# Kernel optimization log

Measured on AMD Instinct MI355X. Metric: run time of the kernel, lower is better.

The kernel has to match this reference:

```python
import jax, jax.numpy as jnp
import numpy as np

D_MODEL = 1024
NUM_HEADS = 16
DEPTH = D_MODEL // NUM_HEADS  # 64
BATCH, SEQ = 4, 2048


def setup_inputs() -> dict:
    key = jax.random.key(0)
    ks = jax.random.split(key, 9)
    s = 1.0 / np.sqrt(D_MODEL)
    x = jax.random.normal(ks[0], (BATCH, SEQ, D_MODEL), dtype=jnp.float32)
    # Per-head Dense weights stacked on a leading head axis [H, d_model, depth]
    Wq = jax.random.normal(ks[1], (NUM_HEADS, D_MODEL, DEPTH), dtype=jnp.float32) * s
    Wk = jax.random.normal(ks[2], (NUM_HEADS, D_MODEL, DEPTH), dtype=jnp.float32) * s
    Wv = jax.random.normal(ks[3], (NUM_HEADS, D_MODEL, DEPTH), dtype=jnp.float32) * s
    bq = jnp.zeros((NUM_HEADS, DEPTH), dtype=jnp.float32)
    bk = jnp.zeros((NUM_HEADS, DEPTH), dtype=jnp.float32)
    bv = jnp.zeros((NUM_HEADS, DEPTH), dtype=jnp.float32)
    Wo = jax.random.normal(ks[4], (D_MODEL, D_MODEL), dtype=jnp.float32) * s
    bo = jnp.zeros((D_MODEL,), dtype=jnp.float32)
    return {"x": x, "Wq": Wq, "bq": bq, "Wk": Wk, "bk": bk,
            "Wv": Wv, "bv": bv, "Wo": Wo, "bo": bo}


def reference(x, Wq, bq, Wk, bk, Wv, bv, Wo, bo):
    # Batched equivalent of the per-head loop: project, attend, concat heads.
    q = jnp.einsum('bsd,hde->bhse', x, Wq) + bq[:, None, :]  # [B,H,S,depth]
    k = jnp.einsum('bsd,hde->bhse', x, Wk) + bk[:, None, :]
    v = jnp.einsum('bsd,hde->bhse', x, Wv) + bv[:, None, :]
    scale = 1.0 / jnp.sqrt(jnp.asarray(DEPTH, dtype=x.dtype))
    scores = jnp.einsum('bhse,bhte->bhst', q, k) * scale      # [B,H,S,S]
    weights = jax.nn.softmax(scores, axis=-1)
    heads = jnp.einsum('bhst,bhte->bhse', weights, v)         # [B,H,S,depth]
    # concat head outputs along last axis in head order (tf.concat axis=-1)
    multi = jnp.transpose(heads, (0, 2, 1, 3)).reshape(x.shape[0], x.shape[1], D_MODEL)
    return multi @ Wo + bo
```

## Files before the change

kernel.cpp:

```cpp
#include <hip/hip_runtime.h>
#include <hip/hip_bf16.h>

#define BATCH 4
#define SEQ   2048
#define DM    1024
#define NH    16
#define DEPTH 64
#define ROWS  (BATCH*SEQ)
#define NQKV  (3*DM)
#define BH    (BATCH*NH)

typedef __attribute__((ext_vector_type(8))) short bf16x8;
typedef __attribute__((ext_vector_type(4))) float f32x4;
typedef __attribute__((ext_vector_type(16))) float f32x16;
typedef unsigned short u16;
typedef unsigned int   u32;

__device__ __forceinline__ u16 f2bf(float f) {
    union { float f; unsigned u; } v; v.f = f;
    unsigned r = v.u + 0x7fff + ((v.u >> 16) & 1);
    return (u16)(r >> 16);
}

__device__ __forceinline__ u32 pk2bf(float a, float b) {
#if __has_builtin(__builtin_amdgcn_cvt_pk_bf16_f32)
    typedef __attribute__((ext_vector_type(2))) __bf16 v2bf;
    union { v2bf v; u32 u; } u_;
    u_.v = __builtin_amdgcn_cvt_pk_bf16_f32(a, b);
    return u_.u;
#else
    return (u32)f2bf(a) | ((u32)f2bf(b) << 16);
#endif
}

__device__ __forceinline__ void plswap(u32 a, u32 b, u32& x, u32& y) {
#if __has_builtin(__builtin_amdgcn_permlane32_swap)
    typedef __attribute__((ext_vector_type(2))) int i32x2;
    i32x2 r = __builtin_amdgcn_permlane32_swap((int)a, (int)b, false, false);
    x = (u32)r.x; y = (u32)r.y;
#else
    u32 as = (u32)__shfl_xor((int)a, 32);
    u32 bs = (u32)__shfl_xor((int)b, 32);
    int h = (threadIdx.x >> 5) & 1;
    x = h ? bs : a;
    y = h ? b : as;
#endif
}

__device__ __forceinline__ void g2l16(void* lds, const void* g) {
    __builtin_amdgcn_global_load_lds((const __attribute__((address_space(1))) void*)g,
                                     (__attribute__((address_space(3))) void*)lds, 16, 0, 0);
}

__device__ __forceinline__ bf16x8 frag8(const u16* tile, int row, int gl) {
    return *(const bf16x8*)(tile + row * 64 + ((gl ^ (row & 7)) * 8));
}

__device__ __forceinline__ f32x16 mfma32(bf16x8 a, bf16x8 b, f32x16 c) {
    return __builtin_amdgcn_mfma_f32_32x32x16_bf16(a, b, c, 0, 0, 0);
}

__global__ __launch_bounds__(256) void k_prep(const float* __restrict__ x,
                                              const float* __restrict__ Wq, const float* __restrict__ Wk,
                                              const float* __restrict__ Wv, const float* __restrict__ Wo,
                                              u16* __restrict__ xb, u16* __restrict__ BT, u16* __restrict__ WoT) {
    __shared__ u16 T[64][65];
    int tid = threadIdx.x;
    int bx = blockIdx.x;
    if (bx < 2048) {
        int i = bx * 4096 + tid * 4;
        for (int l = 0; l < 4; ++l) {
            float4 v = *(const float4*)(x + i + l * 1024);
            ushort4 o; o.x = f2bf(v.x); o.y = f2bf(v.y); o.z = f2bf(v.z); o.w = f2bf(v.w);
            *(ushort4*)(xb + i + l * 1024) = o;
        }
        return;
    }
    if (bx < 2816) {
        int q = bx - 2048;
        int kt = q & 15, mh = q >> 4, m = mh >> 4, h = mh & 15;
        const float* W = (m == 0) ? Wq : (m == 1) ? Wk : Wv;
        const float* src = W + ((size_t)h * 1024 + kt * 64) * 64;
        int e = tid & 63, r0 = tid >> 6;
        for (int i = 0; i < 16; ++i) { int r = i * 4 + r0; T[r][e] = f2bf(src[r * 64 + e]); }
        __syncthreads();
        int kk = tid & 63, e0 = tid >> 6;
        u16* dst = BT + ((size_t)m * 1024 + h * 64) * 1024 + kt * 64;
        for (int i = 0; i < 16; ++i) { int ee = i * 4 + e0; dst[ee * 1024 + kk] = T[kk][ee]; }
        return;
    }
    {
        int q = bx - 2816;
        int kt = q & 15, nt = q >> 4;
        const float* src = Wo + (size_t)kt * 64 * 1024 + nt * 64;
        int c = tid & 63, r0 = tid >> 6;
        for (int i = 0; i < 16; ++i) { int r = i * 4 + r0; T[r][c] = f2bf(src[r * 1024 + c]); }
        __syncthreads();
        int kk = tid & 63, e0 = tid >> 6;
        u16* dst = WoT + (size_t)nt * 64 * 1024 + kt * 64;
        for (int i = 0; i < 16; ++i) { int ee = i * 4 + e0; dst[ee * 1024 + kk] = T[kk][ee]; }
    }
}

__global__ __launch_bounds__(256) void k_gemm_qkv(const u16* __restrict__ xb, const u16* __restrict__ Wt,
                                                  const float* __restrict__ bq, const float* __restrict__ bk,
                                                  const float* __restrict__ bv,
                                                  u16* __restrict__ Q, u16* __restrict__ K, u16* __restrict__ VT) {
    __shared__ u16 Al[128 * 64];
    __shared__ u16 Bl[128 * 64];
    int tid = threadIdx.x;
    int wave = tid >> 6, lane = tid & 63, ln = lane & 15, quad = lane >> 4;
    int b = blockIdx.x;
    bool isvt = (b >= 1024);
    int row0, col0;
    const u16 *Am, *Bm;
    if (!isvt) {
        col0 = (b & 15) * 128; row0 = (b >> 4) * 128;
        Am = xb + (size_t)row0 * 1024; Bm = Wt + (size_t)col0 * 1024;
    } else {
        int b2 = b - 1024;
        col0 = (b2 & 63) * 128; row0 = (b2 >> 6) * 128;
        Am = Wt + (size_t)2048 * 1024 + (size_t)row0 * 1024; Bm = xb + (size_t)col0 * 1024;
    }
    int moff = (wave >> 1) * 64, noff = (wave & 1) * 64;
    f32x4 acc[4][4] = {};

    for (int k0 = 0; k0 < 1024; k0 += 64) {
        for (int l = 0; l < 4; ++l) {
            int idx = tid + l * 256, r = idx >> 3, gs = ((idx & 7) ^ (r & 7)) * 8;
            g2l16(&Al[idx * 8], Am + r * 1024 + k0 + gs);
            g2l16(&Bl[idx * 8], Bm + r * 1024 + k0 + gs);
        }
        __syncthreads();
        for (int kk = 0; kk < 2; ++kk) {
            bf16x8 a[4], bb[4];
            for (int i = 0; i < 4; ++i) a[i]  = frag8(Al, moff + i * 16 + ln, kk * 4 + quad);
            for (int j = 0; j < 4; ++j) bb[j] = frag8(Bl, noff + j * 16 + ln, kk * 4 + quad);
            for (int i = 0; i < 4; ++i)
                for (int j = 0; j < 4; ++j)
                    acc[i][j] = __builtin_amdgcn_mfma_f32_16x16x32_bf16(a[i], bb[j], acc[i][j], 0, 0, 0);
        }
        __syncthreads();
    }

    if (!isvt) {
        const float QSCALE = 0.125f * 1.4426950408889634f;
        for (int j = 0; j < 4; ++j) {
            int c = col0 + noff + j * 16 + ln;
            int m = c >> 10, h = (c >> 6) & 15, e = c & 63;
            const float* bias = (m == 0) ? bq : bk;
            float bval = bias[h * 64 + e];
            for (int i = 0; i < 4; ++i)
                for (int r = 0; r < 4; ++r) {
                    int rowg = row0 + moff + i * 16 + quad * 4 + r;
                    int b_ = rowg >> 11, s = rowg & 2047;
                    int bh = b_ * 16 + h;
                    float v = acc[i][j][r] + bval;
                    if (m == 0) Q[(bh * 2048 + s) * 64 + e] = f2bf(v * QSCALE);
                    else        K[(bh * 2048 + s) * 64 + e] = f2bf(v);
                }
        }
    } else {
        for (int j = 0; j < 4; ++j) {
            int c = col0 + noff + j * 16 + ln;
            int b_ = c >> 11, s = c & 2047;
            for (int i = 0; i < 4; ++i)
                for (int r = 0; r < 4; ++r) {
                    int ii = row0 + moff + i * 16 + quad * 4 + r;
                    float v = acc[i][j][r] + bv[ii];
                    VT[((size_t)b_ * 1024 + ii) * 2048 + s] = f2bf(v);
                }
        }
    }
}

__global__ __launch_bounds__(256, 4) void k_attn(const u16* __restrict__ Q, const u16* __restrict__ K,
                                                 const u16* __restrict__ VT, u16* __restrict__ A2) {
    __shared__ u16 Kl[2][64 * 64];
    __shared__ u16 Vl[2][64 * 64];
    __shared__ float linv[128];
    int tid = threadIdx.x;
    int wave = tid >> 6, lane = tid & 63, l31 = lane & 31, h = lane >> 5;
    int bh = blockIdx.y;
    int m0 = blockIdx.x * 128;
    const u16* Qb = Q + (size_t)bh * 2048 * 64;
    const u16* Kb = K + (size_t)bh * 2048 * 64;
    const u16* Vb = VT + (size_t)bh * 64 * 2048;

    const u16* kp[2]; const u16* vp[2]; int dsti[2];
    for (int l = 0; l < 2; ++l) {
        int idx = tid + l * 256, r = idx >> 3, gs = ((idx & 7) ^ (r & 7)) * 8;
        dsti[l] = idx * 8;
        kp[l] = Kb + r * 64 + gs;
        vp[l] = Vb + r * 2048 + gs;
    }

    bf16x8 qb[4];
    {
        const u16* q0 = Qb + (size_t)(m0 + wave * 32 + l31) * 64 + h * 8;
#pragma unroll
        for (int s = 0; s < 4; ++s) qb[s] = *(const bf16x8*)(q0 + s * 16);
    }

    for (int l = 0; l < 2; ++l) { g2l16(&Kl[0][dsti[l]], kp[l]); g2l16(&Vl[0][dsti[l]], vp[l]); }
    __syncthreads();

    f32x16 oacc[2] = {};
    float lsum = 0.f;

    for (int t = 0; t < 32; ++t) {
        int cur = t & 1;
        if (t < 31) {
            for (int l = 0; l < 2; ++l) {
                g2l16(&Kl[cur ^ 1][dsti[l]], kp[l] + (t + 1) * 4096);
                g2l16(&Vl[cur ^ 1][dsti[l]], vp[l] + (t + 1) * 64);
            }
        }

        f32x16 sc[2] = {};
        __builtin_amdgcn_s_setprio(1);
#pragma unroll
        for (int s = 0; s < 4; ++s) {
            bf16x8 kf0 = frag8(Kl[cur], l31,      2 * s + h);
            bf16x8 kf1 = frag8(Kl[cur], 32 + l31, 2 * s + h);
            sc[0] = mfma32(kf0, qb[s], sc[0]);
            sc[1] = mfma32(kf1, qb[s], sc[1]);
        }
        __builtin_amdgcn_s_setprio(0);

        bf16x8 pa[4];
        float sq = 0.f;
#pragma unroll
        for (int kt = 0; kt < 2; ++kt)
#pragma unroll
            for (int gp = 0; gp < 2; ++gp) {
                float e00 = __builtin_amdgcn_exp2f(sc[kt][(2 * gp) * 4 + 0]);
                float e01 = __builtin_amdgcn_exp2f(sc[kt][(2 * gp) * 4 + 1]);
                float e02 = __builtin_amdgcn_exp2f(sc[kt][(2 * gp) * 4 + 2]);
                float e03 = __builtin_amdgcn_exp2f(sc[kt][(2 * gp) * 4 + 3]);
                float e10 = __builtin_amdgcn_exp2f(sc[kt][(2 * gp + 1) * 4 + 0]);
                float e11 = __builtin_amdgcn_exp2f(sc[kt][(2 * gp + 1) * 4 + 1]);
                float e12 = __builtin_amdgcn_exp2f(sc[kt][(2 * gp + 1) * 4 + 2]);
                float e13 = __builtin_amdgcn_exp2f(sc[kt][(2 * gp + 1) * 4 + 3]);
                sq += ((e00 + e01) + (e02 + e03)) + ((e10 + e11) + (e12 + e13));
                u32 ue = pk2bf(e00, e01), ve = pk2bf(e02, e03);
                u32 uo = pk2bf(e10, e11), vo = pk2bf(e12, e13);
                u32 w0, w1, w2, w3;
                plswap(ue, uo, w0, w2);
                plswap(ve, vo, w1, w3);
                union { bf16x8 v; u32 w[4]; } pu;
                pu.w[0] = w0; pu.w[1] = w1; pu.w[2] = w2; pu.w[3] = w3;
                pa[2 * kt + gp] = pu.v;
            }
        lsum += sq;

        __builtin_amdgcn_s_setprio(1);
#pragma unroll
        for (int s = 0; s < 4; ++s) {
            bf16x8 bv0 = frag8(Vl[cur], l31,      2 * s + h);
            bf16x8 bv1 = frag8(Vl[cur], 32 + l31, 2 * s + h);
            oacc[0] = mfma32(pa[s], bv0, oacc[0]);
            oacc[1] = mfma32(pa[s], bv1, oacc[1]);
        }
        __builtin_amdgcn_s_setprio(0);

        __syncthreads();
    }

    {
        float l2 = lsum + __shfl_xor(lsum, 32);
        linv[wave * 32 + l31] = 1.0f / l2;
    }
    int b_ = bh >> 4, hh = bh & 15;
    for (int g = 0; g < 4; ++g) {
        f32x4 iv = *(f32x4*)&linv[wave * 32 + 8 * g + 4 * h];
        for (int dt = 0; dt < 2; ++dt)
            for (int r = 0; r < 4; ++r) {
                int row = b_ * 2048 + m0 + wave * 32 + 8 * g + 4 * h + r;
                A2[row * 1024 + hh * 64 + dt * 32 + l31] = f2bf(oacc[dt][g * 4 + r] * iv[r]);
            }
    }
}

__global__ __launch_bounds__(256) void k_gemm_out(const u16* __restrict__ A, const u16* __restrict__ BT,
                                                  const float* __restrict__ bo, float* __restrict__ out) {
    __shared__ u16 Al[128 * 64];
    __shared__ u16 Bl[128 * 64];
    int tid = threadIdx.x;
    int wave = tid >> 6, lane = tid & 63, ln = lane & 15, quad = lane >> 4;
    int row0 = blockIdx.y * 128;
    int col0 = blockIdx.x * 128;
    int moff = (wave >> 1) * 64, noff = (wave & 1) * 64;
    f32x4 acc[4][4] = {};

    for (int k0 = 0; k0 < 1024; k0 += 64) {
        for (int l = 0; l < 4; ++l) {
            int idx = tid + l * 256, r = idx >> 3, gs = ((idx & 7) ^ (r & 7)) * 8;
            g2l16(&Al[idx * 8], A  + (row0 + r) * 1024 + k0 + gs);
            g2l16(&Bl[idx * 8], BT + (col0 + r) * 1024 + k0 + gs);
        }
        __syncthreads();
        for (int kk = 0; kk < 2; ++kk) {
            bf16x8 a[4], b[4];
            for (int i = 0; i < 4; ++i) a[i] = frag8(Al, moff + i * 16 + ln, kk * 4 + quad);
            for (int j = 0; j < 4; ++j) b[j] = frag8(Bl, noff + j * 16 + ln, kk * 4 + quad);
            for (int i = 0; i < 4; ++i)
                for (int j = 0; j < 4; ++j)
                    acc[i][j] = __builtin_amdgcn_mfma_f32_16x16x32_bf16(a[i], b[j], acc[i][j], 0, 0, 0);
        }
        __syncthreads();
    }

    for (int j = 0; j < 4; ++j) {
        int c = col0 + noff + j * 16 + ln;
        float bias = bo[c];
        for (int i = 0; i < 4; ++i)
            for (int r = 0; r < 4; ++r) {
                int rowg = row0 + moff + i * 16 + quad * 4 + r;
                out[rowg * 1024 + c] = acc[i][j][r] + bias;
            }
    }
}

extern "C" void kernel_launch(void* const* d_in, const int* in_sizes, int n_in,
                              void* d_out, int out_size, void* d_ws, size_t ws_size,
                              hipStream_t stream) {
    const float* x  = (const float*)d_in[0];
    const float* Wq = (const float*)d_in[1];
    const float* bq = (const float*)d_in[2];
    const float* Wk = (const float*)d_in[3];
    const float* bk = (const float*)d_in[4];
    const float* Wv = (const float*)d_in[5];
    const float* bv = (const float*)d_in[6];
    const float* Wo = (const float*)d_in[7];
    const float* bo = (const float*)d_in[8];
    float* out = (float*)d_out;

    char* ws = (char*)d_ws;
    u16* xb    = (u16*)ws; ws += (size_t)ROWS * DM * 2;
    u16* WqkvT = (u16*)ws; ws += (size_t)NQKV * DM * 2;
    u16* WoT   = (u16*)ws; ws += (size_t)DM * DM * 2;
    u16* Qb    = (u16*)ws; ws += (size_t)BH * SEQ * DEPTH * 2;
    u16* Kb    = (u16*)ws; ws += (size_t)BH * SEQ * DEPTH * 2;
    u16* VTb   = (u16*)ws; ws += (size_t)BH * SEQ * DEPTH * 2;
    u16* A2    = xb;
    (void)ws_size;

    k_prep     <<<dim3(3072),   dim3(256), 0, stream>>>(x, Wq, Wk, Wv, Wo, xb, WqkvT, WoT);
    k_gemm_qkv <<<dim3(1536),   dim3(256), 0, stream>>>(xb, WqkvT, bq, bk, bv, Qb, Kb, VTb);
    k_attn     <<<dim3(16, 64), dim3(256), 0, stream>>>(Qb, Kb, VTb, A2);
    k_gemm_out <<<dim3(8, 64),  dim3(256), 0, stream>>>(A2, WoT, bo, out);
}
```

Measured before the change: 291.4 us.

## Retile QKV and output GEMMs to 256-wide double-buffered 32x32 MFMA blocks

Both projection GEMMs move from 128x128 tiles with 256 threads to 256x256 (QKV) and 256x128 (output) tiles with 512 threads. The K-loop now double-buffers LDS with the next tile's loads issued before the current compute, and it uses 32x32x16 MFMA fragments raised with s_setprio. Block indices are remapped to spread neighbouring tiles across XCDs. The goal is more operand reuse per LDS byte and overlap of global loads with MFMA work. The cost is larger LDS use (128KB or 96KB per block), fewer blocks in flight, and a higher register count.

```diff
diff --git a/kernel.cpp b/kernel.cpp
--- a/kernel.cpp
+++ b/kernel.cpp
@@ -102,72 +102,105 @@
     }
 }
 
-__global__ __launch_bounds__(256) void k_gemm_qkv(const u16* __restrict__ xb, const u16* __restrict__ Wt,
-                                                  const float* __restrict__ bq, const float* __restrict__ bk,
-                                                  const float* __restrict__ bv,
-                                                  u16* __restrict__ Q, u16* __restrict__ K, u16* __restrict__ VT) {
-    __shared__ u16 Al[128 * 64];
-    __shared__ u16 Bl[128 * 64];
+__global__ __launch_bounds__(512, 2) void k_gemm_qkv(const u16* __restrict__ xb, const u16* __restrict__ Wt,
+                                                     const float* __restrict__ bq, const float* __restrict__ bk,
+                                                     const float* __restrict__ bv,
+                                                     u16* __restrict__ Q, u16* __restrict__ K, u16* __restrict__ VT) {
+    __shared__ u16 Al[2][256 * 64];
+    __shared__ u16 Bl[2][256 * 64];
     int tid = threadIdx.x;
-    int wave = tid >> 6, lane = tid & 63, ln = lane & 15, quad = lane >> 4;
+    int wave = tid >> 6, lane = tid & 63, l31 = lane & 31, h2 = lane >> 5;
+    int wr = wave >> 2, wc = wave & 3;
+
     int b = blockIdx.x;
-    bool isvt = (b >= 1024);
+    int wg = (b & 7) * 48 + (b >> 3);
+
+    bool isvt = (wg >= 256);
     int row0, col0;
     const u16 *Am, *Bm;
     if (!isvt) {
-        col0 = (b & 15) * 128; row0 = (b >> 4) * 128;
-        Am = xb + (size_t)row0 * 1024; Bm = Wt + (size_t)col0 * 1024;
+        row0 = (wg >> 3) * 256; col0 = (wg & 7) * 256;
+        Am = xb + (size_t)row0 * 1024;
+        Bm = Wt + (size_t)col0 * 1024;
     } else {
-        int b2 = b - 1024;
-        col0 = (b2 & 63) * 128; row0 = (b2 >> 6) * 128;
-        Am = Wt + (size_t)2048 * 1024 + (size_t)row0 * 1024; Bm = xb + (size_t)col0 * 1024;
-    }
-    int moff = (wave >> 1) * 64, noff = (wave & 1) * 64;
-    f32x4 acc[4][4] = {};
-
-    for (int k0 = 0; k0 < 1024; k0 += 64) {
-        for (int l = 0; l < 4; ++l) {
-            int idx = tid + l * 256, r = idx >> 3, gs = ((idx & 7) ^ (r & 7)) * 8;
-            g2l16(&Al[idx * 8], Am + r * 1024 + k0 + gs);
-            g2l16(&Bl[idx * 8], Bm + r * 1024 + k0 + gs);
-        }
-        __syncthreads();
-        for (int kk = 0; kk < 2; ++kk) {
-            bf16x8 a[4], bb[4];
-            for (int i = 0; i < 4; ++i) a[i]  = frag8(Al, moff + i * 16 + ln, kk * 4 + quad);
-            for (int j = 0; j < 4; ++j) bb[j] = frag8(Bl, noff + j * 16 + ln, kk * 4 + quad);
-            for (int i = 0; i < 4; ++i)
-                for (int j = 0; j < 4; ++j)
-                    acc[i][j] = __builtin_amdgcn_mfma_f32_16x16x32_bf16(a[i], bb[j], acc[i][j], 0, 0, 0);
-        }
+        int b2 = wg - 256;
+        row0 = (b2 >> 5) * 256; col0 = (b2 & 31) * 256;
+        Am = Wt + (size_t)(2048 + row0) * 1024;
+        Bm = xb + (size_t)col0 * 1024;
+    }
+
+    f32x16 acc[4][2] = {};
+
+#pragma unroll
+    for (int l = 0; l < 4; ++l) {
+        int idx = tid + l * 512, r = idx >> 3, gs = ((idx & 7) ^ (r & 7)) * 8;
+        g2l16(&Al[0][idx * 8], Am + r * 1024 + gs);
+        g2l16(&Bl[0][idx * 8], Bm + r * 1024 + gs);
+    }
+    __syncthreads();
+
+    for (int t = 0; t < 16; ++t) {
+        int cur = t & 1;
+        if (t < 15) {
+            int k0 = (t + 1) * 64;
+#pragma unroll
+            for (int l = 0; l < 4; ++l) {
+                int idx = tid + l * 512, r = idx >> 3, gs = ((idx & 7) ^ (r & 7)) * 8;
+                g2l16(&Al[cur ^ 1][idx * 8], Am + r * 1024 + k0 + gs);
+                g2l16(&Bl[cur ^ 1][idx * 8], Bm + r * 1024 + k0 + gs);
+            }
+        }
+        __builtin_amdgcn_s_setprio(1);
+#pragma unroll
+        for (int kk = 0; kk < 4; ++kk) {
+            bf16x8 a[4], bb[2];
+#pragma unroll
+            for (int mi = 0; mi < 4; ++mi) a[mi] = frag8(Al[cur], wr * 128 + mi * 32 + l31, 2 * kk + h2);
+#pragma unroll
+            for (int ni = 0; ni < 2; ++ni) bb[ni] = frag8(Bl[cur], wc * 64 + ni * 32 + l31, 2 * kk + h2);
+#pragma unroll
+            for (int mi = 0; mi < 4; ++mi)
+#pragma unroll
+                for (int ni = 0; ni < 2; ++ni)
+                    acc[mi][ni] = mfma32(a[mi], bb[ni], acc[mi][ni]);
+        }
+        __builtin_amdgcn_s_setprio(0);
         __syncthreads();
     }
 
     if (!isvt) {
         const float QSCALE = 0.125f * 1.4426950408889634f;
-        for (int j = 0; j < 4; ++j) {
-            int c = col0 + noff + j * 16 + ln;
-            int m = c >> 10, h = (c >> 6) & 15, e = c & 63;
-            const float* bias = (m == 0) ? bq : bk;
+        int m = (col0 >= 1024);
+        const float* bias = m ? bk : bq;
+        u16* dst0 = m ? K : Q;
+#pragma unroll
+        for (int ni = 0; ni < 2; ++ni) {
+            int c = col0 + wc * 64 + ni * 32 + l31;
+            int h = (c >> 6) & 15, e = c & 63;
             float bval = bias[h * 64 + e];
-            for (int i = 0; i < 4; ++i)
-                for (int r = 0; r < 4; ++r) {
-                    int rowg = row0 + moff + i * 16 + quad * 4 + r;
+#pragma unroll
+            for (int mi = 0; mi < 4; ++mi)
+#pragma unroll
+                for (int reg = 0; reg < 16; ++reg) {
+                    int rowg = row0 + wr * 128 + mi * 32 + (reg & 3) + 8 * (reg >> 2) + 4 * h2;
                     int b_ = rowg >> 11, s = rowg & 2047;
                     int bh = b_ * 16 + h;
-                    float v = acc[i][j][r] + bval;
-                    if (m == 0) Q[(bh * 2048 + s) * 64 + e] = f2bf(v * QSCALE);
-                    else        K[(bh * 2048 + s) * 64 + e] = f2bf(v);
+                    float v = acc[mi][ni][reg] + bval;
+                    if (!m) v *= QSCALE;
+                    dst0[((size_t)bh * 2048 + s) * 64 + e] = f2bf(v);
                 }
         }
     } else {
-        for (int j = 0; j < 4; ++j) {
-            int c = col0 + noff + j * 16 + ln;
+#pragma unroll
+        for (int ni = 0; ni < 2; ++ni) {
+            int c = col0 + wc * 64 + ni * 32 + l31;
             int b_ = c >> 11, s = c & 2047;
-            for (int i = 0; i < 4; ++i)
-                for (int r = 0; r < 4; ++r) {
-                    int ii = row0 + moff + i * 16 + quad * 4 + r;
-                    float v = acc[i][j][r] + bv[ii];
+#pragma unroll
+            for (int mi = 0; mi < 4; ++mi)
+#pragma unroll
+                for (int reg = 0; reg < 16; ++reg) {
+                    int ii = row0 + wr * 128 + mi * 32 + (reg & 3) + 8 * (reg >> 2) + 4 * h2;
+                    float v = acc[mi][ni][reg] + bv[ii];
                     VT[((size_t)b_ * 1024 + ii) * 2048 + s] = f2bf(v);
                 }
         }
@@ -282,42 +315,66 @@
     }
 }
 
-__global__ __launch_bounds__(256) void k_gemm_out(const u16* __restrict__ A, const u16* __restrict__ BT,
-                                                  const float* __restrict__ bo, float* __restrict__ out) {
-    __shared__ u16 Al[128 * 64];
-    __shared__ u16 Bl[128 * 64];
+__global__ __launch_bounds__(512, 2) void k_gemm_out(const u16* __restrict__ A, const u16* __restrict__ BT,
+                                                     const float* __restrict__ bo, float* __restrict__ out) {
+    __shared__ u16 Al[2][256 * 64];
+    __shared__ u16 Bl[2][128 * 64];
     int tid = threadIdx.x;
-    int wave = tid >> 6, lane = tid & 63, ln = lane & 15, quad = lane >> 4;
-    int row0 = blockIdx.y * 128;
-    int col0 = blockIdx.x * 128;
-    int moff = (wave >> 1) * 64, noff = (wave & 1) * 64;
-    f32x4 acc[4][4] = {};
-
-    for (int k0 = 0; k0 < 1024; k0 += 64) {
-        for (int l = 0; l < 4; ++l) {
-            int idx = tid + l * 256, r = idx >> 3, gs = ((idx & 7) ^ (r & 7)) * 8;
-            g2l16(&Al[idx * 8], A  + (row0 + r) * 1024 + k0 + gs);
-            g2l16(&Bl[idx * 8], BT + (col0 + r) * 1024 + k0 + gs);
-        }
+    int wave = tid >> 6, lane = tid & 63, l31 = lane & 31, h2 = lane >> 5;
+    int wr = wave >> 2, wc = wave & 3;
+
+    int b = blockIdx.x;
+    int wg = (b & 7) * 32 + (b >> 3);
+    int row0 = (wg >> 3) * 256, col0 = (wg & 7) * 128;
+
+    const u16* Am = A  + (size_t)row0 * 1024;
+    const u16* Bm = BT + (size_t)col0 * 1024;
+
+    f32x16 acc[4] = {};
+
+#pragma unroll
+    for (int l = 0; l < 4; ++l) {
+        int idx = tid + l * 512, r = idx >> 3, gs = ((idx & 7) ^ (r & 7)) * 8;
+        g2l16(&Al[0][idx * 8], Am + r * 1024 + gs);
+        if (l < 2) g2l16(&Bl[0][idx * 8], Bm + r * 1024 + gs);
+    }
+    __syncthreads();
+
+    for (int t = 0; t < 16; ++t) {
+        int cur = t & 1;
+        if (t < 15) {
+            int k0 = (t + 1) * 64;
+#pragma unroll
+            for (int l = 0; l < 4; ++l) {
+                int idx = tid + l * 512, r = idx >> 3, gs = ((idx & 7) ^ (r & 7)) * 8;
+                g2l16(&Al[cur ^ 1][idx * 8], Am + r * 1024 + k0 + gs);
+                if (l < 2) g2l16(&Bl[cur ^ 1][idx * 8], Bm + r * 1024 + k0 + gs);
+            }
+        }
+        __builtin_amdgcn_s_setprio(1);
+#pragma unroll
+        for (int kk = 0; kk < 4; ++kk) {
+            bf16x8 a[4], bb;
+#pragma unroll
+            for (int mi = 0; mi < 4; ++mi) a[mi] = frag8(Al[cur], wr * 128 + mi * 32 + l31, 2 * kk + h2);
+            bb = frag8(Bl[cur], wc * 32 + l31, 2 * kk + h2);
+#pragma unroll
+            for (int mi = 0; mi < 4; ++mi)
+                acc[mi] = mfma32(a[mi], bb, acc[mi]);
+        }
+        __builtin_amdgcn_s_setprio(0);
         __syncthreads();
-        for (int kk = 0; kk < 2; ++kk) {
-            bf16x8 a[4], b[4];
-            for (int i = 0; i < 4; ++i) a[i] = frag8(Al, moff + i * 16 + ln, kk * 4 + quad);
-            for (int j = 0; j < 4; ++j) b[j] = frag8(Bl, noff + j * 16 + ln, kk * 4 + quad);
-            for (int i = 0; i < 4; ++i)
-                for (int j = 0; j < 4; ++j)
-                    acc[i][j] = __builtin_amdgcn_mfma_f32_16x16x32_bf16(a[i], b[j], acc[i][j], 0, 0, 0);
-        }
-        __syncthreads();
-    }
-
-    for (int j = 0; j < 4; ++j) {
-        int c = col0 + noff + j * 16 + ln;
+    }
+
+    {
+        int c = col0 + wc * 32 + l31;
         float bias = bo[c];
-        for (int i = 0; i < 4; ++i)
-            for (int r = 0; r < 4; ++r) {
-                int rowg = row0 + moff + i * 16 + quad * 4 + r;
-                out[rowg * 1024 + c] = acc[i][j][r] + bias;
+#pragma unroll
+        for (int mi = 0; mi < 4; ++mi)
+#pragma unroll
+            for (int reg = 0; reg < 16; ++reg) {
+                int rowg = row0 + wr * 128 + mi * 32 + (reg & 3) + 8 * (reg >> 2) + 4 * h2;
+                out[(size_t)rowg * 1024 + c] = acc[mi][reg] + bias;
             }
     }
 }
@@ -347,7 +404,7 @@
     (void)ws_size;
 
     k_prep     <<<dim3(3072),   dim3(256), 0, stream>>>(x, Wq, Wk, Wv, Wo, xb, WqkvT, WoT);
-    k_gemm_qkv <<<dim3(1536),   dim3(256), 0, stream>>>(xb, WqkvT, bq, bk, bv, Qb, Kb, VTb);
+    k_gemm_qkv <<<dim3(384),    dim3(512), 0, stream>>>(xb, WqkvT, bq, bk, bv, Qb, Kb, VTb);
     k_attn     <<<dim3(16, 64), dim3(256), 0, stream>>>(Qb, Kb, VTb, A2);
-    k_gemm_out <<<dim3(8, 64),  dim3(256), 0, stream>>>(A2, WoT, bo, out);
-}
+    k_gemm_out <<<dim3(256),    dim3(512), 0, stream>>>(A2, WoT, bo, out);
+}
```

New measurement: 303.4 us. 4.1% more time.
